# Performance work log

Measured on AMD Instinct MI355X. Metric: run time of the kernel, lower is better.

## Reference

```python
import jax, jax.numpy as jnp
import numpy as np

N, D, C, E, K = 100000, 64, 40, 1600000, 2

def setup_inputs() -> dict:
    key = jax.random.key(0)
    k1, k2, k3 = jax.random.split(key, 3)
    x = jax.random.normal(k1, (N, D), dtype=jnp.float32)
    edge_index = jax.random.randint(k2, (2, E), 0, N, dtype=jnp.int64)
    W = jax.random.normal(k3, (D, C), dtype=jnp.float32) * 0.05
    b = jnp.zeros((C,), dtype=jnp.float32)
    return {"x": x, "edge_index": edge_index, "W": W, "b": b}

def reference(x, edge_index, W, b):
    n = x.shape[0]
    self_loop = jnp.arange(n, dtype=edge_index.dtype)
    row = jnp.concatenate([edge_index[0], self_loop])  # [E+N]
    col = jnp.concatenate([edge_index[1], self_loop])  # [E+N]
    # degree over row (out-degree incl. self loops), as in torch_geometric.utils.degree
    deg = jax.ops.segment_sum(jnp.ones_like(row, dtype=x.dtype), row, num_segments=n)
    deg_inv_sqrt = jnp.where(deg > 0, jax.lax.rsqrt(deg), 0.0)
    norm = deg_inv_sqrt[row] * deg_inv_sqrt[col]  # [E+N]
    # K hops of SpMM: out[r] += norm_e * x[c] for each edge e=(r,c)
    for _ in range(K):
        x = jax.ops.segment_sum(norm[:, None] * x[col], row, num_segments=n)
    logits = x @ W + b  # [N, C]
    return jax.nn.log_softmax(logits, axis=1)
```

## Files before the change

### kernel.cpp

```cpp
#include <hip/hip_runtime.h>
#include <math.h>


#define D_FEAT 64
#define NCLS 40
#define BROWS 512
#define BROWS_LOG 9
#define BINCAP 10240
#define CSRCAP 12288
#define EPT 25

typedef float v2f __attribute__((ext_vector_type(2)));

__device__ __forceinline__ unsigned pack_bf16_2(float lo, float hi) {
    unsigned ulo = __float_as_uint(lo);
    unsigned uhi = __float_as_uint(hi);
    ulo = (ulo + 0x7fffu + ((ulo >> 16) & 1u)) >> 16;
    uhi = (uhi + 0x7fffu + ((uhi >> 16) & 1u)) & 0xffff0000u;
    return uhi | ulo;
}

__device__ __forceinline__ void acc2p(unsigned u, v2f& a) {
    v2f v;
    v.x = __uint_as_float(u << 16);
    v.y = __uint_as_float(u & 0xffff0000u);
    a += v;
}

__global__ __launch_bounds__(256) void bin_edges_kernel(const int* __restrict__ rows,
                                                        const int* __restrict__ cols,
                                                        int* __restrict__ bucket_cursor,
                                                        unsigned* __restrict__ bins,
                                                        int e, int nb) {
    __shared__ int cnt[512];
    for (int i = threadIdx.x; i < nb; i += 256) cnt[i] = 0;
    __syncthreads();
    int base = blockIdx.x * (256 * EPT) + threadIdx.x;
    int rr[EPT], cc[EPT];
#pragma unroll
    for (int k = 0; k < EPT; k++) {
        int idx = base + k * 256;
        if (idx < e) { rr[k] = rows[idx]; cc[k] = cols[idx]; }
        else { rr[k] = -1; cc[k] = 0; }
    }
#pragma unroll
    for (int k = 0; k < EPT; k++)
        if (rr[k] >= 0) atomicAdd(&cnt[rr[k] >> BROWS_LOG], 1);
    __syncthreads();
    for (int i = threadIdx.x; i < nb; i += 256) {
        int c = cnt[i];
        cnt[i] = (c > 0) ? atomicAdd(&bucket_cursor[i], c) : 0;
    }
    __syncthreads();
#pragma unroll
    for (int k = 0; k < EPT; k++) {
        if (rr[k] >= 0) {
            int b = rr[k] >> BROWS_LOG;
            int pos = atomicAdd(&cnt[b], 1);
            bins[(size_t)b * BINCAP + pos] =
                ((unsigned)(rr[k] & (BROWS - 1)) << 17) | (unsigned)cc[k];
        }
    }
}

__global__ __launch_bounds__(512) void build_csr_kernel(const unsigned* __restrict__ bins,
                                                        const int* __restrict__ bucket_cursor,
                                                        int* __restrict__ csr_col,
                                                        uint2* __restrict__ row_info,
                                                        float* __restrict__ dis,
                                                        uint4* __restrict__ pinfo, int n) {
    __shared__ int cnt[512];
    __shared__ int sm[512];
    __shared__ int cur[512];
    __shared__ int lcsr[CSRCAP];
    int b = blockIdx.x;
    int tid = threadIdx.x;
    int m = bucket_cursor[b];
    cnt[tid] = 0;
    __syncthreads();
    const unsigned* bp = bins + (size_t)b * BINCAP;
    for (int i = tid; i < m; i += 512) atomicAdd(&cnt[bp[i] >> 17], 1);
    __syncthreads();
    int c = cnt[tid];
    int padded = (c + 3) & ~3;
    int r = b * BROWS + tid;
    float dv = rsqrtf(1.0f + (float)c);
    if (r < n) dis[r] = dv;
    sm[tid] = padded;
    __syncthreads();
    for (int off = 1; off < 512; off <<= 1) {
        int t = (tid >= off) ? sm[tid - off] : 0;
        __syncthreads();
        sm[tid] += t;
        __syncthreads();
    }
    int off0 = sm[tid] - padded;
    cur[tid] = off0;
    if (r < n) row_info[r] = make_uint2((unsigned)(b * CSRCAP + off0), (unsigned)padded);
    __syncthreads();
    for (int i = tid; i < m; i += 512) {
        unsigned u = bp[i];
        int pos = atomicAdd(&cur[u >> 17], 1);
        lcsr[pos] = (int)(u & 0x1FFFFu);
    }
    __syncthreads();
    if (r < n) {
        for (int j = c; j < padded; j++) lcsr[off0 + j] = n;
    }
    __syncthreads();
    int tot = sm[511];
    int4* cp4 = (int4*)(csr_col + (size_t)b * CSRCAP);
    const int4* l4 = (const int4*)lcsr;
    for (int i = tid; i < (tot >> 2); i += 512) cp4[i] = l4[i];
    {
        int g = tot + tid;
        if (g < CSRCAP) csr_col[(size_t)b * CSRCAP + g] = n;
    }

    __syncthreads();
    if (tid < 64) cnt[tid] = 0;
    __syncthreads();
    int bin = min(padded >> 2, 63);
    if (r < n) atomicAdd(&cnt[bin], 1);
    __syncthreads();
    if (tid < 64) sm[tid] = cnt[tid];
    __syncthreads();
    for (int off = 1; off < 64; off <<= 1) {
        int t = (tid >= off && tid < 64) ? sm[tid - off] : 0;
        __syncthreads();
        if (tid < 64) sm[tid] += t;
        __syncthreads();
    }
    if (tid < 64) cur[tid] = sm[tid] - cnt[tid];
    __syncthreads();
    if (r < n) {
        int rank = atomicAdd(&cur[bin], 1);
        pinfo[b * BROWS + rank] = make_uint4((unsigned)(b * CSRCAP + off0),
                                             (unsigned)padded, (unsigned)r,
                                             __float_as_uint(dv));
    } else {
        pinfo[b * BROWS + tid] = make_uint4(0u, 0u, 0xFFFFFFFFu, 0u);
    }
}

__global__ __launch_bounds__(256) void sort_scale_kernel(int* __restrict__ csr_col,
                                                         const uint2* __restrict__ row_info,
                                                         const float* __restrict__ x,
                                                         const float* __restrict__ dis,
                                                         unsigned* __restrict__ xs0,
                                                         unsigned* __restrict__ xs1,
                                                         int n, int sortBlocks) {
    if ((int)blockIdx.x >= sortBlocks) {
        int i = ((int)blockIdx.x - sortBlocks) * 256 + threadIdx.x;
        int total = (n + 1) * (D_FEAT / 2);
        if (i >= total) return;
        int node = i >> 5;
        if (node < n) {
            float s = dis[node];
            float2 v = ((const float2*)x)[i];
            xs0[i] = pack_bf16_2(s * v.x, s * v.y);
        } else {
            xs0[i] = 0u;
            xs1[i] = 0u;
        }
        return;
    }
    int wid = ((int)blockIdx.x * 256 + (int)threadIdx.x) >> 6;
    int lane = threadIdx.x & 63;
    int r0 = wid * 2, r1 = r0 + 1;
    if (r0 >= n) return;
    uint2 i0 = row_info[r0];
    uint2 i1 = (r1 < n) ? row_info[r1] : make_uint2(0u, 0u);
    int p0 = (int)i0.y, p1 = (int)i1.y;
    if (p0 <= 32 && p1 <= 32) {
        int half = lane >> 5, hl = lane & 31;
        int base = half ? (int)i1.x : (int)i0.x;
        int pad  = half ? p1 : p0;
        int key = (hl < pad) ? csr_col[base + hl] : 0x7fffffff;
#pragma unroll
        for (int k = 2; k <= 32; k <<= 1) {
#pragma unroll
            for (int j = k >> 1; j > 0; j >>= 1) {
                int other = __shfl_xor(key, j, 64);
                bool takeMin = (((hl & j) == 0) == ((hl & k) == 0));
                int mn = min(key, other), mx = max(key, other);
                key = takeMin ? mn : mx;
            }
        }
        if (hl < pad) csr_col[base + hl] = key;
    } else {
        for (int t = 0; t < 2; t++) {
            int base = t ? (int)i1.x : (int)i0.x;
            int pad  = t ? p1 : p0;
            if (pad == 0) continue;
            if (pad <= 64) {
                int key = (lane < pad) ? csr_col[base + lane] : 0x7fffffff;
#pragma unroll
                for (int k = 2; k <= 64; k <<= 1) {
#pragma unroll
                    for (int j = k >> 1; j > 0; j >>= 1) {
                        int other = __shfl_xor(key, j, 64);
                        bool takeMin = (((lane & j) == 0) == ((lane & k) == 0));
                        int mn = min(key, other), mx = max(key, other);
                        key = takeMin ? mn : mx;
                    }
                }
                if (lane < pad) csr_col[base + lane] = key;
            } else if (lane == 0) {
                for (int i2 = 1; i2 < pad; i2++) {
                    int kk = csr_col[base + i2];
                    int j2 = i2 - 1;
                    while (j2 >= 0 && csr_col[base + j2] > kk) {
                        csr_col[base + j2 + 1] = csr_col[base + j2]; j2--;
                    }
                    csr_col[base + j2 + 1] = kk;
                }
            }
        }
    }
}

#define GATHER_ITER(cp, xs_in, ql, base, len)                               \
    uint2 u0 = xs_in[cv0.x * 16 + ql], u1 = xs_in[cv0.y * 16 + ql];         \
    uint2 u2 = xs_in[cv0.z * 16 + ql], u3 = xs_in[cv0.w * 16 + ql];         \
    uint2 u4 = xs_in[cv1.x * 16 + ql], u5 = xs_in[cv1.y * 16 + ql];         \
    uint2 u6 = xs_in[cv1.z * 16 + ql], u7 = xs_in[cv1.w * 16 + ql];         \
    uint2 u8 = xs_in[cv2.x * 16 + ql], u9 = xs_in[cv2.y * 16 + ql];         \
    uint2 u10 = xs_in[cv2.z * 16 + ql], u11 = xs_in[cv2.w * 16 + ql];       \
    uint2 u12 = xs_in[cv3.x * 16 + ql], u13 = xs_in[cv3.y * 16 + ql];       \
    uint2 u14 = xs_in[cv3.z * 16 + ql], u15 = xs_in[cv3.w * 16 + ql];       \
    {                                                                       \
        int nb4 = (base >> 2) + 4;                                          \
        nv0 = cp[nb4]; nv1 = cp[nb4 + 1];                                   \
        nv2 = cp[nb4 + 2]; nv3 = cp[nb4 + 3];                               \
    }                                                                       \
    __builtin_amdgcn_sched_barrier(0);                                      \
    if (base < len) {                                                       \
        acc2p(u0.x, hA01); acc2p(u0.y, hA23);                               \
        acc2p(u1.x, hA01); acc2p(u1.y, hA23);                               \
        acc2p(u2.x, hA01); acc2p(u2.y, hA23);                               \
        acc2p(u3.x, hA01); acc2p(u3.y, hA23);                               \
    }                                                                       \
    if (base + 4 < len) {                                                   \
        acc2p(u4.x, hB01); acc2p(u4.y, hB23);                               \
        acc2p(u5.x, hB01); acc2p(u5.y, hB23);                               \
        acc2p(u6.x, hB01); acc2p(u6.y, hB23);                               \
        acc2p(u7.x, hB01); acc2p(u7.y, hB23);                               \
    }                                                                       \
    if (base + 8 < len) {                                                   \
        acc2p(u8.x, hA01); acc2p(u8.y, hA23);                               \
        acc2p(u9.x, hA01); acc2p(u9.y, hA23);                               \
        acc2p(u10.x, hA01); acc2p(u10.y, hA23);                             \
        acc2p(u11.x, hA01); acc2p(u11.y, hA23);                             \
    }                                                                       \
    if (base + 12 < len) {                                                  \
        acc2p(u12.x, hB01); acc2p(u12.y, hB23);                             \
        acc2p(u13.x, hB01); acc2p(u13.y, hB23);                             \
        acc2p(u14.x, hB01); acc2p(u14.y, hB23);                             \
        acc2p(u15.x, hB01); acc2p(u15.y, hB23);                             \
    }                                                                       \
    cv0 = nv0; cv1 = nv1; cv2 = nv2; cv3 = nv3;

__global__ __launch_bounds__(256, 5) void spmm_hop1_kernel(const uint2* __restrict__ xs_in,
                                                           uint2* __restrict__ xs_out,
                                                           const uint4* __restrict__ pinfo,
                                                           const int* __restrict__ csr_col,
                                                           int n) {
    int wave = (blockIdx.x * blockDim.x + threadIdx.x) >> 6;
    int lane = threadIdx.x & 63;
    int q = lane >> 4, ql = lane & 15;
    uint4 info = pinfo[wave * 4 + q];
    int s = (int)info.x, len = (int)info.y;
    int r = (int)info.z;
    bool valid = (r >= 0);
    int maxlen = len;
    maxlen = max(maxlen, __shfl_xor(maxlen, 16, 64));
    maxlen = max(maxlen, __shfl_xor(maxlen, 32, 64));

    v2f hA01 = {0.f, 0.f}, hA23 = {0.f, 0.f};
    v2f hB01 = {0.f, 0.f}, hB23 = {0.f, 0.f};
    const uint4* cp = (const uint4*)(csr_col + s);
    uint4 cv0 = cp[0], cv1 = cp[1], cv2 = cp[2], cv3 = cp[3];
    uint4 nv0, nv1, nv2, nv3;
    for (int base = 0; base < maxlen; base += 16) {
        GATHER_ITER(cp, xs_in, ql, base, len)
    }
    if (valid) {
        v2f h01 = hA01 + hB01;
        v2f h23 = hA23 + hB23;
        uint2 us = xs_in[r * 16 + ql];
        acc2p(us.x, h01); acc2p(us.y, h23);
        float dr = __uint_as_float(info.w);
        float d2 = dr * dr;
        xs_out[r * 16 + ql] = make_uint2(pack_bf16_2(d2 * h01.x, d2 * h01.y),
                                         pack_bf16_2(d2 * h23.x, d2 * h23.y));
    }
}

__global__ __launch_bounds__(256, 5) void spmm_logits_kernel(const uint2* __restrict__ xs_in,
                                                             const uint4* __restrict__ pinfo,
                                                             const int* __restrict__ csr_col,
                                                             const float* __restrict__ W,
                                                             const float* __restrict__ b,
                                                             float* __restrict__ out,
                                                             int n) {
    __shared__ float Wt[NCLS][D_FEAT + 4];
    __shared__ float bl[NCLS];
    __shared__ float hl[16][D_FEAT + 4];
    for (int i = threadIdx.x; i < D_FEAT * NCLS; i += 256) {
        int d = i / NCLS, cc = i - d * NCLS;
        Wt[cc][d] = W[i];
    }
    for (int i = threadIdx.x; i < NCLS; i += 256) bl[i] = b[i];
    __syncthreads();

    int wave = (blockIdx.x * blockDim.x + threadIdx.x) >> 6;
    int lane = threadIdx.x & 63;
    int q = lane >> 4, ql = lane & 15;
    uint4 info = pinfo[wave * 4 + q];
    int s = (int)info.x, len = (int)info.y;
    int r = (int)info.z;
    bool valid = (r >= 0);
    int maxlen = len;
    maxlen = max(maxlen, __shfl_xor(maxlen, 16, 64));
    maxlen = max(maxlen, __shfl_xor(maxlen, 32, 64));

    v2f hA01 = {0.f, 0.f}, hA23 = {0.f, 0.f};
    v2f hB01 = {0.f, 0.f}, hB23 = {0.f, 0.f};
    const uint4* cp = (const uint4*)(csr_col + s);
    uint4 cv0 = cp[0], cv1 = cp[1], cv2 = cp[2], cv3 = cp[3];
    uint4 nv0, nv1, nv2, nv3;
    for (int base = 0; base < maxlen; base += 16) {
        GATHER_ITER(cp, xs_in, ql, base, len)
    }

    float y0, y1, y2;
    int c0 = ql, c1 = ql + 16;
    int c2 = (ql < 8) ? (ql + 32) : ql;
    {
        v2f h01 = hA01 + hB01;
        v2f h23 = hA23 + hB23;
        uint2 us = valid ? xs_in[r * 16 + ql] : make_uint2(0u, 0u);
        acc2p(us.x, h01); acc2p(us.y, h23);
        float dr = __uint_as_float(info.w);
        float h0 = h01.x * dr, h1 = h01.y * dr, h2 = h23.x * dr, h3 = h23.y * dr;

        int rowslot = ((threadIdx.x >> 6) << 2) + q;
        *(float4*)&hl[rowslot][ql * 4] = make_float4(h0, h1, h2, h3);

        y0 = bl[c0]; y1 = bl[c1]; y2 = bl[c2];
#pragma unroll
        for (int g = 0; g < 16; g++) {
            float4 hv = *(const float4*)&hl[rowslot][g * 4];
            float4 w0 = *(const float4*)&Wt[c0][g * 4];
            float4 w1 = *(const float4*)&Wt[c1][g * 4];
            float4 w2 = *(const float4*)&Wt[c2][g * 4];
            y0 += hv.x * w0.x + hv.y * w0.y + hv.z * w0.z + hv.w * w0.w;
            y1 += hv.x * w1.x + hv.y * w1.y + hv.z * w1.z + hv.w * w1.w;
            y2 += hv.x * w2.x + hv.y * w2.y + hv.z * w2.z + hv.w * w2.w;
        }
    }

    bool has3 = (ql < 8);
    float m = fmaxf(y0, y1);
    if (has3) m = fmaxf(m, y2);
#pragma unroll
    for (int o = 8; o > 0; o >>= 1) m = fmaxf(m, __shfl_xor(m, o, 64));
    float sm = __expf(y0 - m) + __expf(y1 - m) + (has3 ? __expf(y2 - m) : 0.f);
#pragma unroll
    for (int o = 8; o > 0; o >>= 1) sm += __shfl_xor(sm, o, 64);
    float lse = m + __logf(sm);

    if (valid) {
        float* op = out + (long long)r * NCLS;
        op[ql] = y0 - lse;
        op[ql + 16] = y1 - lse;
        if (has3) op[ql + 32] = y2 - lse;
    }
}

extern "C" void kernel_launch(void* const* d_in, const int* in_sizes, int n_in,
                              void* d_out, int out_size, void* d_ws, size_t ws_size,
                              hipStream_t stream) {
    const float* x  = (const float*)d_in[0];
    const int*   ei = (const int*)d_in[1];
    const float* W  = (const float*)d_in[2];
    const float* b  = (const float*)d_in[3];
    float* out = (float*)d_out;

    const int n = in_sizes[0] / D_FEAT;
    const int e = in_sizes[1] / 2;
    const int nb = (n + BROWS - 1) / BROWS;

    const int* rows = ei;
    const int* cols = ei + e;

    size_t na = ((size_t)n + 256) & ~(size_t)255;
    size_t npm = (size_t)nb * BROWS;
    int*      bucket_cursor = (int*)d_ws;
    float*    dis           = (float*)(bucket_cursor + 256);
    uint2*    row_info      = (uint2*)(dis + na);
    uint4*    pinfo         = (uint4*)(row_info + na);
    unsigned* bins          = (unsigned*)(pinfo + npm);
    int*      csr_col       = (int*)(bins + (size_t)nb * BINCAP);
    unsigned* xs0           = (unsigned*)(csr_col + (size_t)nb * CSRCAP);
    unsigned* xs1           = xs0 + (size_t)(n + 1) * (D_FEAT / 2);

    const int BS = 256;

    hipMemsetAsync(bucket_cursor, 0, (size_t)nb * sizeof(int), stream);
    {
        int blocks = (e + BS * EPT - 1) / (BS * EPT);
        bin_edges_kernel<<<blocks, BS, 0, stream>>>(rows, cols, bucket_cursor, bins, e, nb);
    }
    build_csr_kernel<<<nb, 512, 0, stream>>>(bins, bucket_cursor, csr_col, row_info, dis,
                                             pinfo, n);
    {
        int nwv = (n + 1) / 2;
        int sortBlocks = (nwv * 64 + BS - 1) / BS;
        int tot = (n + 1) * (D_FEAT / 2);
        int scaleBlocks = (tot + BS - 1) / BS;
        sort_scale_kernel<<<sortBlocks + scaleBlocks, BS, 0, stream>>>(
            csr_col, row_info, x, dis, xs0, xs1, n, sortBlocks);
    }

    int nwaves = (int)npm / 4;
    int blocks = (nwaves * 64 + BS - 1) / BS;
    spmm_hop1_kernel<<<blocks, BS, 0, stream>>>((const uint2*)xs0, (uint2*)xs1, pinfo,
                                                csr_col, n);
    spmm_logits_kernel<<<blocks, BS, 0, stream>>>((const uint2*)xs1, pinfo, csr_col,
                                                  W, b, out, n);
}
```

Baseline: 213.9 us.

## Apply linear projection before propagation to gather 40-dim rows instead of 64

Reorders the computation so X·W is computed first in a new tiled xw_kernel, scaled by deg^-1/2 and stored as bf16. Both SpMM hops then gather 40-wide (80-byte, five uint4) rows instead of 64-wide rows, which cuts gather traffic. Each wave now processes 12 rows with 5 lanes each, and the final kernel only adds bias and computes log-softmax. The cost is an extra GEMM kernel, a memset of both feature buffers, 4 idle lanes per wave, and different bf16 rounding points.

```diff
diff --git a/kernel.cpp b/kernel.cpp
--- a/kernel.cpp
+++ b/kernel.cpp
@@ -4,11 +4,14 @@
 
 #define D_FEAT 64
 #define NCLS 40
+#define NDW 20
+#define NV4 5
 #define BROWS 512
 #define BROWS_LOG 9
 #define BINCAP 10240
 #define CSRCAP 12288
 #define EPT 25
+#define XW_ROWS 192
 
 typedef float v2f __attribute__((ext_vector_type(2)));
 
@@ -143,29 +146,10 @@
     }
 }
 
-__global__ __launch_bounds__(256) void sort_scale_kernel(int* __restrict__ csr_col,
-                                                         const uint2* __restrict__ row_info,
-                                                         const float* __restrict__ x,
-                                                         const float* __restrict__ dis,
-                                                         unsigned* __restrict__ xs0,
-                                                         unsigned* __restrict__ xs1,
-                                                         int n, int sortBlocks) {
-    if ((int)blockIdx.x >= sortBlocks) {
-        int i = ((int)blockIdx.x - sortBlocks) * 256 + threadIdx.x;
-        int total = (n + 1) * (D_FEAT / 2);
-        if (i >= total) return;
-        int node = i >> 5;
-        if (node < n) {
-            float s = dis[node];
-            float2 v = ((const float2*)x)[i];
-            xs0[i] = pack_bf16_2(s * v.x, s * v.y);
-        } else {
-            xs0[i] = 0u;
-            xs1[i] = 0u;
-        }
-        return;
-    }
-    int wid = ((int)blockIdx.x * 256 + (int)threadIdx.x) >> 6;
+__global__ __launch_bounds__(256) void sort_rows_kernel(int* __restrict__ csr_col,
+                                                        const uint2* __restrict__ row_info,
+                                                        int n) {
+    int wid = (int)((blockIdx.x * blockDim.x + threadIdx.x) >> 6);
     int lane = threadIdx.x & 63;
     int r0 = wid * 2, r1 = r0 + 1;
     if (r0 >= n) return;
@@ -220,162 +204,162 @@
     }
 }
 
-#define GATHER_ITER(cp, xs_in, ql, base, len)                               \
-    uint2 u0 = xs_in[cv0.x * 16 + ql], u1 = xs_in[cv0.y * 16 + ql];         \
-    uint2 u2 = xs_in[cv0.z * 16 + ql], u3 = xs_in[cv0.w * 16 + ql];         \
-    uint2 u4 = xs_in[cv1.x * 16 + ql], u5 = xs_in[cv1.y * 16 + ql];         \
-    uint2 u6 = xs_in[cv1.z * 16 + ql], u7 = xs_in[cv1.w * 16 + ql];         \
-    uint2 u8 = xs_in[cv2.x * 16 + ql], u9 = xs_in[cv2.y * 16 + ql];         \
-    uint2 u10 = xs_in[cv2.z * 16 + ql], u11 = xs_in[cv2.w * 16 + ql];       \
-    uint2 u12 = xs_in[cv3.x * 16 + ql], u13 = xs_in[cv3.y * 16 + ql];       \
-    uint2 u14 = xs_in[cv3.z * 16 + ql], u15 = xs_in[cv3.w * 16 + ql];       \
-    {                                                                       \
-        int nb4 = (base >> 2) + 4;                                          \
-        nv0 = cp[nb4]; nv1 = cp[nb4 + 1];                                   \
-        nv2 = cp[nb4 + 2]; nv3 = cp[nb4 + 3];                               \
-    }                                                                       \
+__global__ __launch_bounds__(192) void xw_kernel(const float* __restrict__ x,
+                                                 const float* __restrict__ W,
+                                                 const float* __restrict__ dis,
+                                                 unsigned* __restrict__ y0, int n) {
+    __shared__ float Xl[XW_ROWS][D_FEAT + 1];
+    __shared__ float Wl[D_FEAT][NCLS + 2];
+    int t = threadIdx.x;
+    int r0 = blockIdx.x * XW_ROWS;
+    for (int i = t; i < D_FEAT * NCLS; i += XW_ROWS) {
+        int d = i / NCLS, c = i - d * NCLS;
+        Wl[d][c] = W[i];
+    }
+    for (int i = t; i < XW_ROWS * D_FEAT; i += XW_ROWS) {
+        int rr = i >> 6, d = i & 63;
+        int r = r0 + rr;
+        Xl[rr][d] = (r < n) ? x[(size_t)r * D_FEAT + d] : 0.f;
+    }
+    __syncthreads();
+    int rq = t >> 2;
+    int cg = t & 3;
+    float acc[4][10];
+#pragma unroll
+    for (int i = 0; i < 4; i++)
+#pragma unroll
+        for (int j = 0; j < 10; j++) acc[i][j] = 0.f;
+#pragma unroll 4
+    for (int d = 0; d < D_FEAT; d++) {
+        float w[10];
+#pragma unroll
+        for (int j = 0; j < 10; j++) w[j] = Wl[d][cg * 10 + j];
+#pragma unroll
+        for (int i = 0; i < 4; i++) {
+            float xv = Xl[rq * 4 + i][d];
+#pragma unroll
+            for (int j = 0; j < 10; j++) acc[i][j] += xv * w[j];
+        }
+    }
+#pragma unroll
+    for (int i = 0; i < 4; i++) {
+        int r = r0 + rq * 4 + i;
+        if (r >= n) continue;
+        float s = dis[r];
+        unsigned* p0 = y0 + (size_t)r * NDW + cg * 5;
+#pragma unroll
+        for (int j = 0; j < 5; j++)
+            p0[j] = pack_bf16_2(s * acc[i][2 * j], s * acc[i][2 * j + 1]);
+    }
+}
+
+#define ACCA(u) acc2p(u.x, h0A); acc2p(u.y, h1A); acc2p(u.z, h2A); acc2p(u.w, h3A);
+#define ACCB(u) acc2p(u.x, h0B); acc2p(u.y, h1B); acc2p(u.z, h2B); acc2p(u.w, h3B);
+#define GATHER8(cp, xs4, gl, base, len)                                     \
+    uint4 cv0 = cp[(base >> 2)], cv1 = cp[(base >> 2) + 1];                 \
+    uint4 u0 = xs4[cv0.x * NV4 + gl], u1 = xs4[cv0.y * NV4 + gl];           \
+    uint4 u2 = xs4[cv0.z * NV4 + gl], u3 = xs4[cv0.w * NV4 + gl];           \
+    uint4 u4 = xs4[cv1.x * NV4 + gl], u5 = xs4[cv1.y * NV4 + gl];           \
+    uint4 u6 = xs4[cv1.z * NV4 + gl], u7 = xs4[cv1.w * NV4 + gl];           \
     __builtin_amdgcn_sched_barrier(0);                                      \
-    if (base < len) {                                                       \
-        acc2p(u0.x, hA01); acc2p(u0.y, hA23);                               \
-        acc2p(u1.x, hA01); acc2p(u1.y, hA23);                               \
-        acc2p(u2.x, hA01); acc2p(u2.y, hA23);                               \
-        acc2p(u3.x, hA01); acc2p(u3.y, hA23);                               \
-    }                                                                       \
-    if (base + 4 < len) {                                                   \
-        acc2p(u4.x, hB01); acc2p(u4.y, hB23);                               \
-        acc2p(u5.x, hB01); acc2p(u5.y, hB23);                               \
-        acc2p(u6.x, hB01); acc2p(u6.y, hB23);                               \
-        acc2p(u7.x, hB01); acc2p(u7.y, hB23);                               \
-    }                                                                       \
-    if (base + 8 < len) {                                                   \
-        acc2p(u8.x, hA01); acc2p(u8.y, hA23);                               \
-        acc2p(u9.x, hA01); acc2p(u9.y, hA23);                               \
-        acc2p(u10.x, hA01); acc2p(u10.y, hA23);                             \
-        acc2p(u11.x, hA01); acc2p(u11.y, hA23);                             \
-    }                                                                       \
-    if (base + 12 < len) {                                                  \
-        acc2p(u12.x, hB01); acc2p(u12.y, hB23);                             \
-        acc2p(u13.x, hB01); acc2p(u13.y, hB23);                             \
-        acc2p(u14.x, hB01); acc2p(u14.y, hB23);                             \
-        acc2p(u15.x, hB01); acc2p(u15.y, hB23);                             \
-    }                                                                       \
-    cv0 = nv0; cv1 = nv1; cv2 = nv2; cv3 = nv3;
-
-__global__ __launch_bounds__(256, 5) void spmm_hop1_kernel(const uint2* __restrict__ xs_in,
-                                                           uint2* __restrict__ xs_out,
+    if (base < len)     { ACCA(u0) ACCA(u1) ACCA(u2) ACCA(u3) }             \
+    if (base + 4 < len) { ACCB(u4) ACCB(u5) ACCB(u6) ACCB(u7) }
+
+__global__ __launch_bounds__(256, 5) void spmm_hop1_kernel(const uint4* __restrict__ xs_in,
+                                                           uint4* __restrict__ xs_out,
                                                            const uint4* __restrict__ pinfo,
                                                            const int* __restrict__ csr_col,
-                                                           int n) {
+                                                           int n, int nperm) {
     int wave = (blockIdx.x * blockDim.x + threadIdx.x) >> 6;
     int lane = threadIdx.x & 63;
-    int q = lane >> 4, ql = lane & 15;
-    uint4 info = pinfo[wave * 4 + q];
-    int s = (int)info.x, len = (int)info.y;
-    int r = (int)info.z;
-    bool valid = (r >= 0);
+    int e = lane / 5;
+    int gl = lane - e * 5;
+    int pidx = wave * 12 + e;
+    bool inb = (e < 12) && (pidx < nperm);
+    uint4 info = pinfo[inb ? pidx : 0];
+    int s = (int)info.x;
+    int len = inb ? (int)info.y : 0;
+    int r = inb ? (int)info.z : -1;
+    float dr = __uint_as_float(inb ? info.w : 0u);
     int maxlen = len;
-    maxlen = max(maxlen, __shfl_xor(maxlen, 16, 64));
-    maxlen = max(maxlen, __shfl_xor(maxlen, 32, 64));
-
-    v2f hA01 = {0.f, 0.f}, hA23 = {0.f, 0.f};
-    v2f hB01 = {0.f, 0.f}, hB23 = {0.f, 0.f};
+#pragma unroll
+    for (int o = 1; o < 64; o <<= 1) maxlen = max(maxlen, __shfl_xor(maxlen, o, 64));
+
+    v2f h0A = {0.f,0.f}, h1A = {0.f,0.f}, h2A = {0.f,0.f}, h3A = {0.f,0.f};
+    v2f h0B = {0.f,0.f}, h1B = {0.f,0.f}, h2B = {0.f,0.f}, h3B = {0.f,0.f};
     const uint4* cp = (const uint4*)(csr_col + s);
-    uint4 cv0 = cp[0], cv1 = cp[1], cv2 = cp[2], cv3 = cp[3];
-    uint4 nv0, nv1, nv2, nv3;
-    for (int base = 0; base < maxlen; base += 16) {
-        GATHER_ITER(cp, xs_in, ql, base, len)
-    }
-    if (valid) {
-        v2f h01 = hA01 + hB01;
-        v2f h23 = hA23 + hB23;
-        uint2 us = xs_in[r * 16 + ql];
-        acc2p(us.x, h01); acc2p(us.y, h23);
-        float dr = __uint_as_float(info.w);
+    for (int base = 0; base < maxlen; base += 8) {
+        GATHER8(cp, xs_in, gl, base, len)
+    }
+    if (r >= 0 && r < n) {
+        v2f h0 = h0A + h0B, h1 = h1A + h1B, h2 = h2A + h2B, h3 = h3A + h3B;
+        uint4 us = xs_in[r * NV4 + gl];
+        acc2p(us.x, h0); acc2p(us.y, h1); acc2p(us.z, h2); acc2p(us.w, h3);
         float d2 = dr * dr;
-        xs_out[r * 16 + ql] = make_uint2(pack_bf16_2(d2 * h01.x, d2 * h01.y),
-                                         pack_bf16_2(d2 * h23.x, d2 * h23.y));
-    }
-}
-
-__global__ __launch_bounds__(256, 5) void spmm_logits_kernel(const uint2* __restrict__ xs_in,
+        uint4 o;
+        o.x = pack_bf16_2(d2 * h0.x, d2 * h0.y);
+        o.y = pack_bf16_2(d2 * h1.x, d2 * h1.y);
+        o.z = pack_bf16_2(d2 * h2.x, d2 * h2.y);
+        o.w = pack_bf16_2(d2 * h3.x, d2 * h3.y);
+        xs_out[r * NV4 + gl] = o;
+    }
+}
+
+__global__ __launch_bounds__(256, 5) void spmm_logits_kernel(const uint4* __restrict__ xs_in,
                                                              const uint4* __restrict__ pinfo,
                                                              const int* __restrict__ csr_col,
-                                                             const float* __restrict__ W,
                                                              const float* __restrict__ b,
                                                              float* __restrict__ out,
-                                                             int n) {
-    __shared__ float Wt[NCLS][D_FEAT + 4];
-    __shared__ float bl[NCLS];
-    __shared__ float hl[16][D_FEAT + 4];
-    for (int i = threadIdx.x; i < D_FEAT * NCLS; i += 256) {
-        int d = i / NCLS, cc = i - d * NCLS;
-        Wt[cc][d] = W[i];
-    }
-    for (int i = threadIdx.x; i < NCLS; i += 256) bl[i] = b[i];
-    __syncthreads();
-
+                                                             int n, int nperm) {
     int wave = (blockIdx.x * blockDim.x + threadIdx.x) >> 6;
     int lane = threadIdx.x & 63;
-    int q = lane >> 4, ql = lane & 15;
-    uint4 info = pinfo[wave * 4 + q];
-    int s = (int)info.x, len = (int)info.y;
-    int r = (int)info.z;
-    bool valid = (r >= 0);
+    int e = lane / 5;
+    int gl = lane - e * 5;
+    int pidx = wave * 12 + e;
+    bool inb = (e < 12) && (pidx < nperm);
+    uint4 info = pinfo[inb ? pidx : 0];
+    int s = (int)info.x;
+    int len = inb ? (int)info.y : 0;
+    int r = inb ? (int)info.z : -1;
+    float dr = __uint_as_float(inb ? info.w : 0u);
     int maxlen = len;
-    maxlen = max(maxlen, __shfl_xor(maxlen, 16, 64));
-    maxlen = max(maxlen, __shfl_xor(maxlen, 32, 64));
-
-    v2f hA01 = {0.f, 0.f}, hA23 = {0.f, 0.f};
-    v2f hB01 = {0.f, 0.f}, hB23 = {0.f, 0.f};
+#pragma unroll
+    for (int o = 1; o < 64; o <<= 1) maxlen = max(maxlen, __shfl_xor(maxlen, o, 64));
+
+    v2f h0A = {0.f,0.f}, h1A = {0.f,0.f}, h2A = {0.f,0.f}, h3A = {0.f,0.f};
+    v2f h0B = {0.f,0.f}, h1B = {0.f,0.f}, h2B = {0.f,0.f}, h3B = {0.f,0.f};
     const uint4* cp = (const uint4*)(csr_col + s);
-    uint4 cv0 = cp[0], cv1 = cp[1], cv2 = cp[2], cv3 = cp[3];
-    uint4 nv0, nv1, nv2, nv3;
-    for (int base = 0; base < maxlen; base += 16) {
-        GATHER_ITER(cp, xs_in, ql, base, len)
-    }
-
-    float y0, y1, y2;
-    int c0 = ql, c1 = ql + 16;
-    int c2 = (ql < 8) ? (ql + 32) : ql;
-    {
-        v2f h01 = hA01 + hB01;
-        v2f h23 = hA23 + hB23;
-        uint2 us = valid ? xs_in[r * 16 + ql] : make_uint2(0u, 0u);
-        acc2p(us.x, h01); acc2p(us.y, h23);
-        float dr = __uint_as_float(info.w);
-        float h0 = h01.x * dr, h1 = h01.y * dr, h2 = h23.x * dr, h3 = h23.y * dr;
-
-        int rowslot = ((threadIdx.x >> 6) << 2) + q;
-        *(float4*)&hl[rowslot][ql * 4] = make_float4(h0, h1, h2, h3);
-
-        y0 = bl[c0]; y1 = bl[c1]; y2 = bl[c2];
-#pragma unroll
-        for (int g = 0; g < 16; g++) {
-            float4 hv = *(const float4*)&hl[rowslot][g * 4];
-            float4 w0 = *(const float4*)&Wt[c0][g * 4];
-            float4 w1 = *(const float4*)&Wt[c1][g * 4];
-            float4 w2 = *(const float4*)&Wt[c2][g * 4];
-            y0 += hv.x * w0.x + hv.y * w0.y + hv.z * w0.z + hv.w * w0.w;
-            y1 += hv.x * w1.x + hv.y * w1.y + hv.z * w1.z + hv.w * w1.w;
-            y2 += hv.x * w2.x + hv.y * w2.y + hv.z * w2.z + hv.w * w2.w;
-        }
-    }
-
-    bool has3 = (ql < 8);
-    float m = fmaxf(y0, y1);
-    if (has3) m = fmaxf(m, y2);
-#pragma unroll
-    for (int o = 8; o > 0; o >>= 1) m = fmaxf(m, __shfl_xor(m, o, 64));
-    float sm = __expf(y0 - m) + __expf(y1 - m) + (has3 ? __expf(y2 - m) : 0.f);
-#pragma unroll
-    for (int o = 8; o > 0; o >>= 1) sm += __shfl_xor(sm, o, 64);
-    float lse = m + __logf(sm);
-
-    if (valid) {
-        float* op = out + (long long)r * NCLS;
-        op[ql] = y0 - lse;
-        op[ql + 16] = y1 - lse;
-        if (has3) op[ql + 32] = y2 - lse;
+    for (int base = 0; base < maxlen; base += 8) {
+        GATHER8(cp, xs_in, gl, base, len)
+    }
+    v2f h0 = h0A + h0B, h1 = h1A + h1B, h2 = h2A + h2B, h3 = h3A + h3B;
+    uint4 us = (r >= 0 && r < n) ? xs_in[r * NV4 + gl] : make_uint4(0u, 0u, 0u, 0u);
+    acc2p(us.x, h0); acc2p(us.y, h1); acc2p(us.z, h2); acc2p(us.w, h3);
+
+    const float4* b4 = (const float4*)b;
+    float4 ba = b4[gl * 2], bb = b4[gl * 2 + 1];
+    float y0 = dr * h0.x + ba.x, y1 = dr * h0.y + ba.y;
+    float y2 = dr * h1.x + ba.z, y3 = dr * h1.y + ba.w;
+    float y4 = dr * h2.x + bb.x, y5 = dr * h2.y + bb.y;
+    float y6 = dr * h3.x + bb.z, y7 = dr * h3.y + bb.w;
+
+    int gb = ((e < 12) ? e : 11) * 5;
+    float mloc = fmaxf(fmaxf(fmaxf(y0, y1), fmaxf(y2, y3)),
+                       fmaxf(fmaxf(y4, y5), fmaxf(y6, y7)));
+    float M = mloc;
+#pragma unroll
+    for (int k = 0; k < 5; k++) M = fmaxf(M, __shfl(mloc, gb + k, 64));
+    float sloc = __expf(y0 - M) + __expf(y1 - M) + __expf(y2 - M) + __expf(y3 - M) +
+                 __expf(y4 - M) + __expf(y5 - M) + __expf(y6 - M) + __expf(y7 - M);
+    float S = 0.f;
+#pragma unroll
+    for (int k = 0; k < 5; k++) S += __shfl(sloc, gb + k, 64);
+    float lse = M + __logf(S);
+
+    if (r >= 0 && r < n) {
+        float4* op = (float4*)(out + (size_t)r * NCLS) + gl * 2;
+        op[0] = make_float4(y0 - lse, y1 - lse, y2 - lse, y3 - lse);
+        op[1] = make_float4(y4 - lse, y5 - lse, y6 - lse, y7 - lse);
     }
 }
 
@@ -403,12 +387,13 @@
     uint4*    pinfo         = (uint4*)(row_info + na);
     unsigned* bins          = (unsigned*)(pinfo + npm);
     int*      csr_col       = (int*)(bins + (size_t)nb * BINCAP);
-    unsigned* xs0           = (unsigned*)(csr_col + (size_t)nb * CSRCAP);
-    unsigned* xs1           = xs0 + (size_t)(n + 1) * (D_FEAT / 2);
+    unsigned* y0            = (unsigned*)(csr_col + (size_t)nb * CSRCAP);
+    unsigned* y1            = y0 + (size_t)(n + 1) * NDW;
 
     const int BS = 256;
 
     hipMemsetAsync(bucket_cursor, 0, (size_t)nb * sizeof(int), stream);
+    hipMemsetAsync(y0, 0, (size_t)(n + 1) * NDW * sizeof(unsigned) * 2, stream);
     {
         int blocks = (e + BS * EPT - 1) / (BS * EPT);
         bin_edges_kernel<<<blocks, BS, 0, stream>>>(rows, cols, bucket_cursor, bins, e, nb);
@@ -418,16 +403,18 @@
     {
         int nwv = (n + 1) / 2;
         int sortBlocks = (nwv * 64 + BS - 1) / BS;
-        int tot = (n + 1) * (D_FEAT / 2);
-        int scaleBlocks = (tot + BS - 1) / BS;
-        sort_scale_kernel<<<sortBlocks + scaleBlocks, BS, 0, stream>>>(
-            csr_col, row_info, x, dis, xs0, xs1, n, sortBlocks);
-    }
-
-    int nwaves = (int)npm / 4;
-    int blocks = (nwaves * 64 + BS - 1) / BS;
-    spmm_hop1_kernel<<<blocks, BS, 0, stream>>>((const uint2*)xs0, (uint2*)xs1, pinfo,
-                                                csr_col, n);
-    spmm_logits_kernel<<<blocks, BS, 0, stream>>>((const uint2*)xs1, pinfo, csr_col,
-                                                  W, b, out, n);
-}
+        sort_rows_kernel<<<sortBlocks, BS, 0, stream>>>(csr_col, row_info, n);
+    }
+    {
+        int tiles = (n + XW_ROWS - 1) / XW_ROWS;
+        xw_kernel<<<tiles, XW_ROWS, 0, stream>>>(x, W, dis, y0, n);
+    }
+
+    int nperm = (int)npm;
+    int nwaves = (nperm + 11) / 12;
+    int blocks = (nwaves + 3) / 4;
+    spmm_hop1_kernel<<<blocks, BS, 0, stream>>>((const uint4*)y0, (uint4*)y1, pinfo,
+                                                csr_col, n, nperm);
+    spmm_logits_kernel<<<blocks, BS, 0, stream>>>((const uint4*)y1, pinfo, csr_col,
+                                                  b, out, n, nperm);
+}
```

Result: slower. 264.0 us (+23.4%).
